# Optimization experiments

Hardware: AMD Instinct MI355X
Metric: run time of the kernel (lower is better)

## Reference

```python
import jax, jax.numpy as jnp
import numpy as np

N_NODES = 100000


def gcn_conv(h, row, col, deg_inv_sqrt, W, b, n_nodes):
    # h: [N, F_in]; PyG GCNConv: linear first, then normalized scatter-add aggregation
    h = h @ W  # [N, F_out]
    norm = deg_inv_sqrt[row] * deg_inv_sqrt[col]  # [E']
    msg = h[row] * norm[:, None]  # gather + scale, [E', F_out]
    out = jax.ops.segment_sum(msg, col, num_segments=n_nodes)  # scatter-add
    return out + b


def setup_inputs() -> dict:
    key = jax.random.key(0)
    ks = jax.random.split(key, 8)
    x = jax.random.normal(ks[0], (N_NODES, 1), dtype=jnp.float32)
    edge_index = jax.random.randint(ks[1], (2, 3200000), 0, N_NODES, dtype=jnp.int64)
    W1 = jax.random.normal(ks[2], (1, 64), dtype=jnp.float32) * 0.5
    b1 = jax.random.normal(ks[3], (64,), dtype=jnp.float32) * 0.1
    W2 = jax.random.normal(ks[4], (64, 32), dtype=jnp.float32) * 0.125
    b2 = jax.random.normal(ks[5], (32,), dtype=jnp.float32) * 0.1
    W3 = jax.random.normal(ks[6], (32, 1), dtype=jnp.float32) * 0.18
    b3 = jax.random.normal(ks[7], (1,), dtype=jnp.float32) * 0.1
    return {"x": x, "edge_index": edge_index, "W1": W1, "b1": b1,
            "W2": W2, "b2": b2, "W3": W3, "b3": b3}


def reference(x, edge_index, W1, b1, W2, b2, W3, b3):
    n = x.shape[0]
    # add self-loops (PyG GCNConv default)
    loops = jnp.arange(n, dtype=edge_index.dtype)
    row = jnp.concatenate([edge_index[0], loops])  # source
    col = jnp.concatenate([edge_index[1], loops])  # target
    # symmetric normalization: deg computed on target nodes with unit edge weight
    deg = jax.ops.segment_sum(jnp.ones_like(col, dtype=x.dtype), col, num_segments=n)
    deg_inv_sqrt = jnp.where(deg > 0, jax.lax.rsqrt(deg), 0.0)

    h = jax.nn.relu(gcn_conv(x, row, col, deg_inv_sqrt, W1, b1, n))
    h = jax.nn.relu(gcn_conv(h, row, col, deg_inv_sqrt, W2, b2, n))
    h = gcn_conv(h, row, col, deg_inv_sqrt, W3, b3, n)  # [N, 1]
    return jax.nn.sigmoid(jnp.sum(h, axis=0))  # [1]
```

## Files before the change

kernel.cpp:

```cpp
#include <hip/hip_runtime.h>
#include <math.h>


#define TB 256
#define TBC 1024
#define TBS 512
#define NPB 128
#define NBMAX 1024
#define CHUNK 8192
#define NCHMAX 512
#define CAPB 6144
#define P8SCALE 64.0f
#define P8INV (1.0f / 64.0f)

__global__ void k_init(const int* __restrict__ ei, int* __restrict__ flag,
                       int* __restrict__ tot, int NB, float* __restrict__ accum) {
    __shared__ int any_nonzero;
    int t = threadIdx.x;
    if (t == 0) any_nonzero = 0;
    __syncthreads();
    if (t < 128) {
        if (ei[2 * t + 1] != 0) atomicOr(&any_nonzero, 1);
    }
    __syncthreads();
    if (t == 0) { flag[0] = (any_nonzero == 0) ? 1 : 0; accum[0] = 0.f; }
    for (int i = t; i < NB; i += blockDim.x) tot[i] = 0;
}

__global__ __launch_bounds__(TBC) void k_chunksort(
        const int* __restrict__ ei, int E, const int* __restrict__ flag,
        unsigned* __restrict__ sbin, unsigned short* __restrict__ s16,
        int* __restrict__ tot, int NB, int nstride) {
    __shared__ int hist[NBMAX];
    __shared__ int cur[NBMAX];
    __shared__ unsigned stage[CHUNK];
    int t = threadIdx.x;
    int sh = flag[0];
    int c0 = blockIdx.x * CHUNK;
    int c1 = min(c0 + CHUNK, E);
    int n = c1 - c0;
    for (int i = t; i < NB; i += TBC) hist[i] = 0;
    __syncthreads();
    for (int e = c0 + t; e < c1; e += TBC) {
        int c = ei[(size_t)(E + e) << sh];
        atomicAdd(&hist[c >> 7], 1);
    }
    __syncthreads();
    int v = (t < NB) ? hist[t] : 0;
    cur[t] = v;
    __syncthreads();
    for (int d = 1; d < TBC; d <<= 1) {
        int a = (t >= d) ? cur[t - d] : 0;
        __syncthreads();
        cur[t] += a;
        __syncthreads();
    }
    int excl = cur[t] - v;
    cur[t] = excl;
    if (t < NB) {
        s16[(size_t)blockIdx.x * nstride + t] = (unsigned short)excl;
        if (v) atomicAdd(&tot[t], v);
    }
    if (t == 0) s16[(size_t)blockIdx.x * nstride + NB] = (unsigned short)n;
    __syncthreads();
    for (int e = c0 + t; e < c1; e += TBC) {
        int r = ei[(size_t)e << sh];
        int c = ei[(size_t)(E + e) << sh];
        int rank = atomicAdd(&cur[c >> 7], 1);
        stage[rank] = ((unsigned)(c & 127) << 17) | (unsigned)r;
    }
    __syncthreads();
    unsigned* dst = sbin + (size_t)blockIdx.x * CHUNK;
    for (int i = t; i < n; i += TBC) dst[i] = stage[i];
}

__global__ void k_scanbins(const int* __restrict__ tot, int* __restrict__ binoff,
                           int NB, int E) {
    __shared__ int s[NBMAX];
    int t = threadIdx.x;
    int v = (t < NB) ? tot[t] : 0;
    s[t] = v;
    __syncthreads();
    for (int d = 1; d < NBMAX; d <<= 1) {
        int a = (t >= d) ? s[t - d] : 0;
        __syncthreads();
        s[t] += a;
        __syncthreads();
    }
    if (t < NB) binoff[t] = s[t] - v;
    if (t == 0) binoff[NB] = E;
}

__global__ __launch_bounds__(TBS) void k_binsort(
        const unsigned* __restrict__ sbin, const unsigned short* __restrict__ s16,
        const int* __restrict__ binoff, int* __restrict__ srow,
        int* __restrict__ off, int* __restrict__ deg,
        const float* __restrict__ x, float* __restrict__ dis,
        float* __restrict__ y, int N, int nchunk, int nstride) {
    __shared__ unsigned stage[CAPB];
    __shared__ int cst[NCHMAX];
    __shared__ int hist[NPB], pfx[NPB];
    int b = blockIdx.x, t = threadIdx.x;
    int b0 = b << 7;
    int nn = min(NPB, N - b0);
    int s0v = 0, v = 0;
    if (t < nchunk) {
        s0v = (int)s16[(size_t)t * nstride + b];
        v = (int)s16[(size_t)t * nstride + b + 1] - s0v;
    }
    cst[t] = v;
    __syncthreads();
    for (int d = 1; d < TBS; d <<= 1) {
        int a = (t >= d) ? cst[t - d] : 0;
        __syncthreads();
        cst[t] += a;
        __syncthreads();
    }
    int myexcl = cst[t] - v;
    if (t < nchunk && v > 0 && myexcl < CAPB) {
        int vc = min(v, CAPB - myexcl);
        const unsigned* src = sbin + (size_t)t * CHUNK + s0v;
        for (int i = 0; i < vc; ++i) stage[myexcl + i] = src[i];
    }
    int bo = binoff[b];
    int cntE = min(binoff[b + 1] - bo, CAPB);
    if (t < NPB) hist[t] = 0;
    __syncthreads();
    for (int i = t; i < cntE; i += TBS) atomicAdd(&hist[stage[i] >> 17], 1);
    __syncthreads();
    int hv = 0;
    if (t < NPB) { hv = hist[t]; pfx[t] = hv; }
    __syncthreads();
    for (int d = 1; d < NPB; d <<= 1) {
        int a = (t < NPB && t >= d) ? pfx[t - d] : 0;
        __syncthreads();
        if (t < NPB) pfx[t] += a;
        __syncthreads();
    }
    int nexcl = (t < NPB) ? (pfx[t] - hv) : 0;
    if (t < nn) {
        int node = b0 + t;
        off[node] = bo + nexcl;
        deg[node] = hv;
        float dd = rsqrtf((float)(hv + 1));
        dis[node] = dd;
        y[node] = x[node] * dd;
    }
    __syncthreads();
    if (t < NPB) hist[t] = nexcl;
    __syncthreads();
    for (int i = t; i < cntE; i += TBS) {
        unsigned pk = stage[i];
        int rank = atomicAdd(&hist[pk >> 17], 1);
        srow[bo + rank] = (int)(pk & 0x1FFFF);
    }
}

__global__ __launch_bounds__(TB) void k_layer1(
        const int* __restrict__ off, const int* __restrict__ deg,
        const int* __restrict__ srow, const float* __restrict__ y,
        const float* __restrict__ dis,
        const float* __restrict__ W1, const float* __restrict__ b1,
        const float* __restrict__ W2, unsigned* __restrict__ p8, int N) {
    __shared__ float sW1[64], sb1[64];
    __shared__ float4 sW2[512];
    for (int k = threadIdx.x; k < 64; k += TB) { sW1[k] = W1[k]; sb1[k] = b1[k]; }
    const float4* W2v = (const float4*)W2;
    for (int k = threadIdx.x; k < 512; k += TB) sW2[k] = W2v[k];
    __syncthreads();

    int c = blockIdx.x * TB + threadIdx.x;
    if (c >= N) return;
    int k0 = off[c], nd = deg[c];
    float s_ = 0.f;
    for (int k = 0; k < nd; ++k) s_ += y[srow[k0 + k]];
    float d = dis[c];
    s_ = (s_ + y[c]) * d;

    float4 g[8];
#pragma unroll
    for (int jj = 0; jj < 8; ++jj) g[jj] = make_float4(0.f, 0.f, 0.f, 0.f);
    for (int f = 0; f < 64; ++f) {
        float hf = fmaxf(fmaf(s_, sW1[f], sb1[f]), 0.f);
#pragma unroll
        for (int jj = 0; jj < 8; ++jj) {
            float4 w = sW2[f * 8 + jj];
            g[jj].x = fmaf(hf, w.x, g[jj].x);
            g[jj].y = fmaf(hf, w.y, g[jj].y);
            g[jj].z = fmaf(hf, w.z, g[jj].z);
            g[jj].w = fmaf(hf, w.w, g[jj].w);
        }
    }
    float sc = d * P8SCALE;
    unsigned pk[8];
#pragma unroll
    for (int jj = 0; jj < 8; ++jj) {
        unsigned u = 0;
        u = __builtin_amdgcn_cvt_pk_fp8_f32(g[jj].x * sc, g[jj].y * sc, u, false);
        u = __builtin_amdgcn_cvt_pk_fp8_f32(g[jj].z * sc, g[jj].w * sc, u, true);
        pk[jj] = u;
    }
    uint4* pv = (uint4*)&p8[(size_t)c * 8];
    pv[0] = make_uint4(pk[0], pk[1], pk[2], pk[3]);
    pv[1] = make_uint4(pk[4], pk[5], pk[6], pk[7]);
}

__global__ __launch_bounds__(TB) void k_layer2(
        const int* __restrict__ off, const int* __restrict__ deg,
        const int* __restrict__ srow, const unsigned* __restrict__ p8,
        const float* __restrict__ dis, const float* __restrict__ b2,
        const float* __restrict__ W3, float* __restrict__ q, int N) {
    int w = (blockIdx.x * TB + threadIdx.x) >> 6;
    int lane = threadIdx.x & 63;
    int grp = lane >> 3;
    int l8 = lane & 7;
    float a0 = 0.f, a1 = 0.f, a2 = 0.f, a3 = 0.f;
    int k0 = 0, nd = 0;
    if (w < N) { k0 = off[w]; nd = deg[w]; }
    for (int k = grp; k < nd; k += 8) {
        int r = srow[k0 + k];
        unsigned v = p8[(size_t)r * 8 + l8];
        auto lo = __builtin_amdgcn_cvt_pk_f32_fp8(v, false);
        auto hi = __builtin_amdgcn_cvt_pk_f32_fp8(v, true);
        a0 += lo[0]; a1 += lo[1]; a2 += hi[0]; a3 += hi[1];
    }
    a0 += __shfl_down(a0, 32); a1 += __shfl_down(a1, 32);
    a2 += __shfl_down(a2, 32); a3 += __shfl_down(a3, 32);
    a0 += __shfl_down(a0, 16); a1 += __shfl_down(a1, 16);
    a2 += __shfl_down(a2, 16); a3 += __shfl_down(a3, 16);
    a0 += __shfl_down(a0, 8);  a1 += __shfl_down(a1, 8);
    a2 += __shfl_down(a2, 8);  a3 += __shfl_down(a3, 8);
    float prod = 0.f;
    float d = (w < N) ? dis[w] : 0.f;
    if (w < N && lane < 8) {
        unsigned v = p8[(size_t)w * 8 + l8];
        auto lo = __builtin_amdgcn_cvt_pk_f32_fp8(v, false);
        auto hi = __builtin_amdgcn_cvt_pk_f32_fp8(v, true);
        float4 b2v = ((const float4*)b2)[l8];
        float4 w3v = ((const float4*)W3)[l8];
        float z0 = fmaf(d, (a0 + lo[0]) * P8INV, b2v.x);
        float z1 = fmaf(d, (a1 + lo[1]) * P8INV, b2v.y);
        float z2 = fmaf(d, (a2 + hi[0]) * P8INV, b2v.z);
        float z3 = fmaf(d, (a3 + hi[1]) * P8INV, b2v.w);
        prod = fmaxf(z0, 0.f) * w3v.x + fmaxf(z1, 0.f) * w3v.y
             + fmaxf(z2, 0.f) * w3v.z + fmaxf(z3, 0.f) * w3v.w;
    }
    prod += __shfl_down(prod, 4);
    prod += __shfl_down(prod, 2);
    prod += __shfl_down(prod, 1);
    if (w < N && lane == 0) q[w] = prod * d;
}

__global__ __launch_bounds__(TB) void k_final(
        const int* __restrict__ off, const int* __restrict__ deg,
        const int* __restrict__ srow, const float* __restrict__ q,
        const float* __restrict__ dis, int N, float* __restrict__ accum) {
    __shared__ float red[TB];
    int c = blockIdx.x * TB + threadIdx.x;
    float v = 0.f;
    if (c < N) {
        int k0 = off[c], nd = deg[c];
        float s = q[c];
        for (int k = 0; k < nd; ++k) s += q[srow[k0 + k]];
        v = s * dis[c];
    }
    red[threadIdx.x] = v;
    __syncthreads();
    for (int d2 = TB / 2; d2 > 0; d2 >>= 1) {
        if (threadIdx.x < d2) red[threadIdx.x] += red[threadIdx.x + d2];
        __syncthreads();
    }
    if (threadIdx.x == 0) atomicAdd(accum, red[0]);
}

__global__ void k_out(const float* __restrict__ accum, const float* __restrict__ b3,
                      float* __restrict__ out, float Nf) {
    float z = accum[0] + Nf * b3[0];
    out[0] = 1.f / (1.f + expf(-z));
}

extern "C" void kernel_launch(void* const* d_in, const int* in_sizes, int n_in,
                              void* d_out, int out_size, void* d_ws, size_t ws_size,
                              hipStream_t stream) {
    const float* x  = (const float*)d_in[0];
    const int*   ei = (const int*)d_in[1];
    const float* W1 = (const float*)d_in[2];
    const float* b1 = (const float*)d_in[3];
    const float* W2 = (const float*)d_in[4];
    const float* b2 = (const float*)d_in[5];
    const float* W3 = (const float*)d_in[6];
    const float* b3 = (const float*)d_in[7];
    float* out = (float*)d_out;

    const int N = in_sizes[0];
    const int E = in_sizes[1] / 2;
    if (N > (1 << 17)) return;
    const int NB = (N + NPB - 1) >> 7;
    const int nchunk = (E + CHUNK - 1) / CHUNK;
    const int nstride = NB + 1;
    if (NB > NBMAX || nchunk > NCHMAX || nchunk > TBS) return;

    char* w = (char*)d_ws;
    size_t o = 0;
    auto alloc = [&](size_t bytes) -> void* {
        void* ptr = w + o;
        o += (bytes + 255) & ~(size_t)255;
        return ptr;
    };
    int*            flag   = (int*)     alloc(256);
    float*          accum  = (float*)   alloc(256);
    int*            tot    = (int*)     alloc((size_t)NBMAX * 4);
    int*            binoff = (int*)     alloc((size_t)(NBMAX + 1) * 4);
    int*            off    = (int*)     alloc((size_t)N * 4);
    int*            deg    = (int*)     alloc((size_t)N * 4);
    float*          dis    = (float*)   alloc((size_t)N * 4);
    float*          y      = (float*)   alloc((size_t)N * 4);
    float*          q      = (float*)   alloc((size_t)N * 4);
    unsigned*       sbin   = (unsigned*)alloc((size_t)nchunk * CHUNK * 4);
    unsigned short* s16    = (unsigned short*)alloc((size_t)nchunk * nstride * 2);
    int*            srow   = (int*)     alloc(((size_t)E + 64) * 4);
    unsigned*       p8     = (unsigned*)alloc((size_t)N * 32);
    if (o > ws_size) return;

    const int nbN = (N + TB - 1) / TB;

    k_init<<<1, 1024, 0, stream>>>(ei, flag, tot, NB, accum);
    k_chunksort<<<nchunk, TBC, 0, stream>>>(ei, E, flag, sbin, s16, tot, NB, nstride);
    k_scanbins<<<1, NBMAX, 0, stream>>>(tot, binoff, NB, E);
    k_binsort<<<NB, TBS, 0, stream>>>(sbin, s16, binoff, srow, off, deg, x, dis, y, N, nchunk, nstride);
    k_layer1<<<nbN, TB, 0, stream>>>(off, deg, srow, y, dis, W1, b1, W2, p8, N);
    k_layer2<<<(N * 64 + TB - 1) / TB, TB, 0, stream>>>(off, deg, srow, p8, dis, b2, W3, q, N);
    k_final<<<nbN, TB, 0, stream>>>(off, deg, srow, q, dis, N, accum);
    k_out<<<1, 1, 0, stream>>>(accum, b3, out, (float)N);
}
```

Before: 190.7 us.

## Use wave-shuffle block scans and wave-per-node gathers in layer2 and final

Swaps the barrier-heavy Hillis-Steele shared-memory scans in chunksort, scanbins and binsort for a shuffle-based warp scan plus a small cross-wave scan. Layer1's neighbor gather is unrolled by four with independent accumulators to raise memory-level parallelism. Layer2 now loads 64 neighbor indices coalesced per wave and broadcasts them with shuffles. k_final moves from one thread per node to one wave per node with a shuffle reduction. The wave-per-node final pass launches 64x more threads for about 32 edges per node, so many lanes sit idle.

```diff
diff --git a/kernel.cpp b/kernel.cpp
--- a/kernel.cpp
+++ b/kernel.cpp
@@ -13,6 +13,30 @@
 #define P8SCALE 64.0f
 #define P8INV (1.0f / 64.0f)
 
+__device__ inline int block_scan_incl(int v, int t, int nthreads, int* wsums) {
+#pragma unroll
+    for (int d = 1; d < 64; d <<= 1) {
+        int n = __shfl_up(v, d);
+        if ((t & 63) >= d) v += n;
+    }
+    int wid = t >> 6;
+    if ((t & 63) == 63) wsums[wid] = v;
+    __syncthreads();
+    if (wid == 0) {
+        int nw = nthreads >> 6;
+        int s = (t < nw) ? wsums[t] : 0;
+#pragma unroll
+        for (int d = 1; d < 16; d <<= 1) {
+            int n = __shfl_up(s, d);
+            if (t >= d) s += n;
+        }
+        if (t < nw) wsums[t] = s;
+    }
+    __syncthreads();
+    if (wid > 0) v += wsums[wid - 1];
+    return v;
+}
+
 __global__ void k_init(const int* __restrict__ ei, int* __restrict__ flag,
                        int* __restrict__ tot, int NB, float* __restrict__ accum) {
     __shared__ int any_nonzero;
@@ -34,6 +58,7 @@
     __shared__ int hist[NBMAX];
     __shared__ int cur[NBMAX];
     __shared__ unsigned stage[CHUNK];
+    __shared__ int wsums[TBC / 64];
     int t = threadIdx.x;
     int sh = flag[0];
     int c0 = blockIdx.x * CHUNK;
@@ -47,15 +72,8 @@
     }
     __syncthreads();
     int v = (t < NB) ? hist[t] : 0;
-    cur[t] = v;
-    __syncthreads();
-    for (int d = 1; d < TBC; d <<= 1) {
-        int a = (t >= d) ? cur[t - d] : 0;
-        __syncthreads();
-        cur[t] += a;
-        __syncthreads();
-    }
-    int excl = cur[t] - v;
+    int incl = block_scan_incl(v, t, TBC, wsums);
+    int excl = incl - v;
     cur[t] = excl;
     if (t < NB) {
         s16[(size_t)blockIdx.x * nstride + t] = (unsigned short)excl;
@@ -76,18 +94,11 @@
 
 __global__ void k_scanbins(const int* __restrict__ tot, int* __restrict__ binoff,
                            int NB, int E) {
-    __shared__ int s[NBMAX];
+    __shared__ int wsums[1024 / 64];
     int t = threadIdx.x;
     int v = (t < NB) ? tot[t] : 0;
-    s[t] = v;
-    __syncthreads();
-    for (int d = 1; d < NBMAX; d <<= 1) {
-        int a = (t >= d) ? s[t - d] : 0;
-        __syncthreads();
-        s[t] += a;
-        __syncthreads();
-    }
-    if (t < NB) binoff[t] = s[t] - v;
+    int incl = block_scan_incl(v, t, 1024, wsums);
+    if (t < NB) binoff[t] = incl - v;
     if (t == 0) binoff[NB] = E;
 }
 
@@ -98,8 +109,8 @@
         const float* __restrict__ x, float* __restrict__ dis,
         float* __restrict__ y, int N, int nchunk, int nstride) {
     __shared__ unsigned stage[CAPB];
-    __shared__ int cst[NCHMAX];
-    __shared__ int hist[NPB], pfx[NPB];
+    __shared__ int hist[NPB];
+    __shared__ int wsums[TBS / 64];
     int b = blockIdx.x, t = threadIdx.x;
     int b0 = b << 7;
     int nn = min(NPB, N - b0);
@@ -108,15 +119,8 @@
         s0v = (int)s16[(size_t)t * nstride + b];
         v = (int)s16[(size_t)t * nstride + b + 1] - s0v;
     }
-    cst[t] = v;
-    __syncthreads();
-    for (int d = 1; d < TBS; d <<= 1) {
-        int a = (t >= d) ? cst[t - d] : 0;
-        __syncthreads();
-        cst[t] += a;
-        __syncthreads();
-    }
-    int myexcl = cst[t] - v;
+    int incl = block_scan_incl(v, t, TBS, wsums);
+    int myexcl = incl - v;
     if (t < nchunk && v > 0 && myexcl < CAPB) {
         int vc = min(v, CAPB - myexcl);
         const unsigned* src = sbin + (size_t)t * CHUNK + s0v;
@@ -128,16 +132,9 @@
     __syncthreads();
     for (int i = t; i < cntE; i += TBS) atomicAdd(&hist[stage[i] >> 17], 1);
     __syncthreads();
-    int hv = 0;
-    if (t < NPB) { hv = hist[t]; pfx[t] = hv; }
-    __syncthreads();
-    for (int d = 1; d < NPB; d <<= 1) {
-        int a = (t < NPB && t >= d) ? pfx[t - d] : 0;
-        __syncthreads();
-        if (t < NPB) pfx[t] += a;
-        __syncthreads();
-    }
-    int nexcl = (t < NPB) ? (pfx[t] - hv) : 0;
+    int hv = (t < NPB) ? hist[t] : 0;
+    int hincl = block_scan_incl(hv, t, TBS, wsums);
+    int nexcl = hincl - hv;
     if (t < nn) {
         int node = b0 + t;
         off[node] = bo + nexcl;
@@ -172,10 +169,16 @@
     int c = blockIdx.x * TB + threadIdx.x;
     if (c >= N) return;
     int k0 = off[c], nd = deg[c];
-    float s_ = 0.f;
-    for (int k = 0; k < nd; ++k) s_ += y[srow[k0 + k]];
+    float s0 = 0.f, s1 = 0.f, s2 = 0.f, s3 = 0.f;
+    int k = 0;
+    for (; k + 4 <= nd; k += 4) {
+        int r0 = srow[k0 + k], r1 = srow[k0 + k + 1];
+        int r2 = srow[k0 + k + 2], r3 = srow[k0 + k + 3];
+        s0 += y[r0]; s1 += y[r1]; s2 += y[r2]; s3 += y[r3];
+    }
+    for (; k < nd; ++k) s0 += y[srow[k0 + k]];
     float d = dis[c];
-    s_ = (s_ + y[c]) * d;
+    float s_ = ((s0 + s1) + (s2 + s3) + y[c]) * d;
 
     float4 g[8];
 #pragma unroll
@@ -215,14 +218,21 @@
     int grp = lane >> 3;
     int l8 = lane & 7;
     float a0 = 0.f, a1 = 0.f, a2 = 0.f, a3 = 0.f;
-    int k0 = 0, nd = 0;
-    if (w < N) { k0 = off[w]; nd = deg[w]; }
-    for (int k = grp; k < nd; k += 8) {
-        int r = srow[k0 + k];
-        unsigned v = p8[(size_t)r * 8 + l8];
-        auto lo = __builtin_amdgcn_cvt_pk_f32_fp8(v, false);
-        auto hi = __builtin_amdgcn_cvt_pk_f32_fp8(v, true);
-        a0 += lo[0]; a1 += lo[1]; a2 += hi[0]; a3 += hi[1];
+    if (w < N) {
+        int k0 = off[w], nd = deg[w];
+        for (int base = 0; base < nd; base += 64) {
+            int m = min(64, nd - base);
+            int idx = 0;
+            if (lane < m) idx = srow[k0 + base + lane];
+#pragma unroll 2
+            for (int i = grp; i < m; i += 8) {
+                int r = __shfl(idx, i);
+                unsigned v = p8[(size_t)r * 8 + l8];
+                auto lo = __builtin_amdgcn_cvt_pk_f32_fp8(v, false);
+                auto hi = __builtin_amdgcn_cvt_pk_f32_fp8(v, true);
+                a0 += lo[0]; a1 += lo[1]; a2 += hi[0]; a3 += hi[1];
+            }
+        }
     }
     a0 += __shfl_down(a0, 32); a1 += __shfl_down(a1, 32);
     a2 += __shfl_down(a2, 32); a3 += __shfl_down(a3, 32);
@@ -255,22 +265,24 @@
         const int* __restrict__ off, const int* __restrict__ deg,
         const int* __restrict__ srow, const float* __restrict__ q,
         const float* __restrict__ dis, int N, float* __restrict__ accum) {
-    __shared__ float red[TB];
-    int c = blockIdx.x * TB + threadIdx.x;
-    float v = 0.f;
-    if (c < N) {
-        int k0 = off[c], nd = deg[c];
-        float s = q[c];
-        for (int k = 0; k < nd; ++k) s += q[srow[k0 + k]];
-        v = s * dis[c];
-    }
-    red[threadIdx.x] = v;
-    __syncthreads();
-    for (int d2 = TB / 2; d2 > 0; d2 >>= 1) {
-        if (threadIdx.x < d2) red[threadIdx.x] += red[threadIdx.x + d2];
-        __syncthreads();
-    }
-    if (threadIdx.x == 0) atomicAdd(accum, red[0]);
+    __shared__ float red[TB / 64];
+    int w = (blockIdx.x * TB + threadIdx.x) >> 6;
+    int lane = threadIdx.x & 63;
+    float s = 0.f;
+    if (w < N) {
+        int k0 = off[w], nd = deg[w];
+        for (int base = 0; base < nd; base += 64) {
+            if (base + lane < nd) s += q[srow[k0 + base + lane]];
+        }
+    }
+    s += __shfl_down(s, 32); s += __shfl_down(s, 16); s += __shfl_down(s, 8);
+    s += __shfl_down(s, 4);  s += __shfl_down(s, 2);  s += __shfl_down(s, 1);
+    if (lane == 0) red[threadIdx.x >> 6] = (w < N) ? dis[w] * (q[w] + s) : 0.f;
+    __syncthreads();
+    if (threadIdx.x == 0) {
+        float t = red[0] + red[1] + red[2] + red[3];
+        atomicAdd(accum, t);
+    }
 }
 
 __global__ void k_out(const float* __restrict__ accum, const float* __restrict__ b3,
@@ -323,13 +335,14 @@
     if (o > ws_size) return;
 
     const int nbN = (N + TB - 1) / TB;
+    const int nbWave = (N * 64 + TB - 1) / TB;
 
     k_init<<<1, 1024, 0, stream>>>(ei, flag, tot, NB, accum);
     k_chunksort<<<nchunk, TBC, 0, stream>>>(ei, E, flag, sbin, s16, tot, NB, nstride);
-    k_scanbins<<<1, NBMAX, 0, stream>>>(tot, binoff, NB, E);
+    k_scanbins<<<1, 1024, 0, stream>>>(tot, binoff, NB, E);
     k_binsort<<<NB, TBS, 0, stream>>>(sbin, s16, binoff, srow, off, deg, x, dis, y, N, nchunk, nstride);
     k_layer1<<<nbN, TB, 0, stream>>>(off, deg, srow, y, dis, W1, b1, W2, p8, N);
-    k_layer2<<<(N * 64 + TB - 1) / TB, TB, 0, stream>>>(off, deg, srow, p8, dis, b2, W3, q, N);
-    k_final<<<nbN, TB, 0, stream>>>(off, deg, srow, q, dis, N, accum);
+    k_layer2<<<nbWave, TB, 0, stream>>>(off, deg, srow, p8, dis, b2, W3, q, N);
+    k_final<<<nbWave, TB, 0, stream>>>(off, deg, srow, q, dis, N, accum);
     k_out<<<1, 1, 0, stream>>>(accum, b3, out, (float)N);
 }
```

New measurement: 460.4 us. 141% more time.
